# Optimization experiments

Measured on AMD Instinct MI355X. Metric: run time of the kernel, lower is better.

Reference implementation:

```python
import math
import jax, jax.numpy as jnp
import numpy as np

N_HEADS = 8
WINDOW = 4


def _get_relative_embeddings(emb, length, window):
    # emb: [1, 2*window+1, k_channels] -> [1, 2*length-1, k_channels]
    pad_length = max(length - (window + 1), 0)
    start = max(window + 1 - length, 0)
    if pad_length > 0:
        emb = jnp.pad(emb, ((0, 0), (pad_length, pad_length), (0, 0)))
    return emb[:, start:start + 2 * length - 1]


def _relative_position_to_absolute_position(x):
    # x: [b, h, l, 2l-1] -> [b, h, l, l] (skewing trick)
    b, h, l, _ = x.shape
    x = jnp.pad(x, ((0, 0), (0, 0), (0, 0), (0, 1)))
    x_flat = x.reshape(b, h, l * 2 * l)
    x_flat = jnp.pad(x_flat, ((0, 0), (0, 0), (0, l - 1)))
    return x_flat.reshape(b, h, l + 1, 2 * l - 1)[:, :, :l, l - 1:]


def _absolute_position_to_relative_position(x):
    # x: [b, h, l, l] -> [b, h, l, 2l-1]
    b, h, l, _ = x.shape
    x = jnp.pad(x, ((0, 0), (0, 0), (0, 0), (0, l - 1)))
    x_flat = x.reshape(b, h, l * l + l * (l - 1))
    x_flat = jnp.pad(x_flat, ((0, 0), (0, 0), (l, 0)))
    return x_flat.reshape(b, h, l, 2 * l)[:, :, :, 1:]


def setup_inputs() -> dict:
    key = jax.random.key(0)
    ks = jax.random.split(key, 12)
    b, t, d = 4, 1024, 512
    kc = d // N_HEADS
    s = 1.0 / math.sqrt(d)
    return {
        "x": jax.random.normal(ks[0], (b, t, d), jnp.float32),
        "c": jax.random.normal(ks[1], (b, t, d), jnp.float32),
        "wq": jax.random.normal(ks[2], (d, d), jnp.float32) * s,
        "bq": jnp.zeros((d,), jnp.float32),
        "wk": jax.random.normal(ks[3], (d, d), jnp.float32) * s,
        "bk": jnp.zeros((d,), jnp.float32),
        "wv": jax.random.normal(ks[4], (d, d), jnp.float32) * s,
        "bv": jnp.zeros((d,), jnp.float32),
        "wo": jax.random.normal(ks[5], (d, d), jnp.float32) * s,
        "bo": jnp.zeros((d,), jnp.float32),
        "emb_rel_k": jax.random.normal(ks[6], (1, 2 * WINDOW + 1, kc), jnp.float32) * kc ** -0.5,
        "emb_rel_v": jax.random.normal(ks[7], (1, 2 * WINDOW + 1, kc), jnp.float32) * kc ** -0.5,
    }


def reference(x, c, wq, bq, wk, bk, wv, bv, wo, bo, emb_rel_k, emb_rel_v):
    b, t, d = x.shape
    h = N_HEADS
    kc = d // h
    inv_sqrt = 1.0 / math.sqrt(kc)

    # 1x1 conv projections (pointwise matmul)
    q = x @ wq + bq   # [b, t, d]
    k = c @ wk + bk
    v = c @ wv + bv

    # Faithful reshape as in source: [b, t, d] -> [b, h, kc, t] -> [b, h, t, kc]
    q = q.reshape(b, h, kc, t).transpose(0, 1, 3, 2)
    k = k.reshape(b, h, kc, t).transpose(0, 1, 3, 2)
    v = v.reshape(b, h, kc, t).transpose(0, 1, 3, 2)

    scores = jnp.einsum('bhtd,bhsd->bhts', q, k) * inv_sqrt  # [b,h,t,t]

    # relative key logits
    key_rel = _get_relative_embeddings(emb_rel_k, t, WINDOW)[0]  # [2t-1, kc]
    rel_logits = jnp.einsum('bhtd,md->bhtm', q, key_rel)          # [b,h,t,2t-1]
    scores_local = _relative_position_to_absolute_position(rel_logits) * inv_sqrt
    scores = scores + scores_local

    p_attn = jax.nn.softmax(scores, axis=-1)
    output = jnp.einsum('bhts,bhsd->bhtd', p_attn, v)  # [b,h,t,kc]

    # relative value contribution
    rel_weights = _absolute_position_to_relative_position(p_attn)  # [b,h,t,2t-1]
    val_rel = _get_relative_embeddings(emb_rel_v, t, WINDOW)[0]    # [2t-1, kc]
    output = output + jnp.einsum('bhtm,md->bhtd', rel_weights, val_rel)

    # Faithful output reshape: [b,h,t,kc] -> [b,h,kc,t] -> [b,t,d]
    output = output.transpose(0, 1, 3, 2).reshape(b, t, d)
    out = output @ wo + bo
    return out
```

## Files before the change

kernel.cpp:

```cpp
#include <hip/hip_runtime.h>
#include <hip/hip_bf16.h>

#define NB 4
#define NT 1024
#define ND 512
#define NH 8
#define NKC 64

typedef __bf16 bf16x8 __attribute__((ext_vector_type(8)));
typedef float f32x4 __attribute__((ext_vector_type(4)));

__device__ __forceinline__ f32x4 MFMA(bf16x8 a, bf16x8 b, f32x4 c) {
    return __builtin_amdgcn_mfma_f32_16x16x32_bf16(a, b, c, 0, 0, 0);
}
__device__ __forceinline__ unsigned short f2bu(float v) {
    __hip_bfloat16 b = __float2bfloat16(v);
    return *(unsigned short*)&b;
}
__device__ __forceinline__ void split1(float v, unsigned short& h, unsigned short& l)
{
    __hip_bfloat16 hb = __float2bfloat16(v);
    float r = v - __bfloat162float(hb);
    __hip_bfloat16 lb = __float2bfloat16(r);
    h = *(unsigned short*)&hb;
    l = *(unsigned short*)&lb;
}
__device__ __forceinline__ void splitpack(const float4 a, const float4 b, uint4& h, uint4& l)
{
    union { unsigned short u[8]; uint4 v; } H, L;
    const float f[8] = {a.x, a.y, a.z, a.w, b.x, b.y, b.z, b.w};
    #pragma unroll
    for (int j = 0; j < 8; ++j) split1(f[j], H.u[j], L.u[j]);
    h = H.v; l = L.v;
}

__global__ __launch_bounds__(256)
void splitT_kernel(const float* __restrict__ w0, const float* __restrict__ w1,
                   const float* __restrict__ w2, const float* __restrict__ w3,
                   unsigned short* __restrict__ wT)
{
    __shared__ float tl[32][33];
    const float* w = (blockIdx.z == 0) ? w0 : (blockIdx.z == 1) ? w1
                   : (blockIdx.z == 2) ? w2 : w3;
    unsigned short* hi = wT + (size_t)blockIdx.z * 2 * (ND * ND);
    unsigned short* lo = hi + ND * ND;
    const int t = threadIdx.x;
    const int x0 = blockIdx.x * 32, y0 = blockIdx.y * 32;
    {
        const int r = t >> 3, c = (t & 7) * 4;
        const float4 v = *(const float4*)&w[(size_t)(y0 + r) * ND + x0 + c];
        tl[r][c] = v.x; tl[r][c+1] = v.y; tl[r][c+2] = v.z; tl[r][c+3] = v.w;
    }
    __syncthreads();
    {
        const int nr = t >> 3, k4 = (t & 7) * 4;
        unsigned short hh[4], ll[4];
        #pragma unroll
        for (int j = 0; j < 4; ++j) split1(tl[k4 + j][nr], hh[j], ll[j]);
        ushort4 h = make_ushort4(hh[0], hh[1], hh[2], hh[3]);
        ushort4 l = make_ushort4(ll[0], ll[1], ll[2], ll[3]);
        *(ushort4*)&hi[(size_t)(x0 + nr) * ND + y0 + k4] = h;
        *(ushort4*)&lo[(size_t)(x0 + nr) * ND + y0 + k4] = l;
    }
}

__global__ __launch_bounds__(256, 3)
void proj_mfma(const float* __restrict__ x, const float* __restrict__ cc,
               const unsigned short* __restrict__ wT,
               const float* __restrict__ bq, const float* __restrict__ bk,
               const float* __restrict__ bv,
               unsigned short* __restrict__ qh_o, unsigned short* __restrict__ ql_o,
               unsigned short* __restrict__ kh_o, unsigned short* __restrict__ vh_o)
{
    __shared__ unsigned short smem[12288];
    unsigned short* Ah = smem;
    unsigned short* Al = smem + 2048;
    unsigned short* Bh = smem + 4096;
    unsigned short* Bl = smem + 8192;
    unsigned short* Tr = smem;

    const int which = blockIdx.z;
    const float* A_g = (which == 0) ? x : cc;
    const unsigned short* Bh_g = wT + (size_t)which * 2 * (ND * ND);
    const unsigned short* Bl_g = Bh_g + ND * ND;
    const float* bias = (which == 0) ? bq : (which == 1) ? bk : bv;

    const int tid = threadIdx.x, l = tid & 63, w = tid >> 6;
    const int quad = l >> 4, lc = l & 15;
    const int wm = w & 1, wn = w >> 1;
    const int n0 = blockIdx.x * 128, m0 = blockIdx.y * 64;

    const int am = tid >> 2, ak = (tid & 3) * 8;
    const size_t aG = (size_t)(m0 + am) * ND + ak;
    const int bn = tid >> 1, bk2 = (tid & 1) * 16;
    const size_t bG = (size_t)(n0 + bn) * ND + bk2;

    float4 ra0 = *(const float4*)&A_g[aG];
    float4 ra1 = *(const float4*)&A_g[aG + 4];
    uint4 rb0 = *(const uint4*)&Bh_g[bG];
    uint4 rb1 = *(const uint4*)&Bh_g[bG + 8];
    uint4 rb2 = {}, rb3 = {};
    if (which != 2) {
        rb2 = *(const uint4*)&Bl_g[bG];
        rb3 = *(const uint4*)&Bl_g[bG + 8];
    }

    f32x4 acc[2][4];
    #pragma unroll
    for (int mi = 0; mi < 2; ++mi)
        #pragma unroll
        for (int ni = 0; ni < 4; ++ni) acc[mi][ni] = (f32x4){0.f, 0.f, 0.f, 0.f};

    for (int k0 = 0; k0 < ND; k0 += 32) {
        __syncthreads();
        {
            uint4 h0, l0;
            splitpack(ra0, ra1, h0, l0);
            *(uint4*)&Ah[am * 32 + ak] = h0;
            *(uint4*)&Al[am * 32 + ak] = l0;
            *(uint4*)&Bh[bn * 32 + bk2] = rb0; *(uint4*)&Bh[bn * 32 + bk2 + 8] = rb1;
            if (which != 2) {
                *(uint4*)&Bl[bn * 32 + bk2] = rb2; *(uint4*)&Bl[bn * 32 + bk2 + 8] = rb3;
            }
        }
        __syncthreads();
        if (k0 + 32 < ND) {
            const size_t aN = aG + k0 + 32, bN = bG + k0 + 32;
            ra0 = *(const float4*)&A_g[aN];
            ra1 = *(const float4*)&A_g[aN + 4];
            rb0 = *(const uint4*)&Bh_g[bN];
            rb1 = *(const uint4*)&Bh_g[bN + 8];
            if (which != 2) {
                rb2 = *(const uint4*)&Bl_g[bN];
                rb3 = *(const uint4*)&Bl_g[bN + 8];
            }
        }

        bf16x8 ah[2], al2[2], bh[4], bl[4];
        #pragma unroll
        for (int mi = 0; mi < 2; ++mi) {
            const int ar = (wm * 32 + mi * 16 + lc) * 32 + quad * 8;
            ah[mi] = *(const bf16x8*)&Ah[ar];
            al2[mi] = *(const bf16x8*)&Al[ar];
        }
        #pragma unroll
        for (int ni = 0; ni < 4; ++ni) {
            const int br = (wn * 64 + ni * 16 + lc) * 32 + quad * 8;
            bh[ni] = *(const bf16x8*)&Bh[br];
            if (which != 2) bl[ni] = *(const bf16x8*)&Bl[br];
        }
        if (which != 2) {
            #pragma unroll
            for (int mi = 0; mi < 2; ++mi)
                #pragma unroll
                for (int ni = 0; ni < 4; ++ni) {
                    acc[mi][ni] = MFMA(al2[mi], bh[ni], acc[mi][ni]);
                    acc[mi][ni] = MFMA(ah[mi], bl[ni], acc[mi][ni]);
                    acc[mi][ni] = MFMA(ah[mi], bh[ni], acc[mi][ni]);
                }
        } else {
            #pragma unroll
            for (int mi = 0; mi < 2; ++mi)
                #pragma unroll
                for (int ni = 0; ni < 4; ++ni) {
                    acc[mi][ni] = MFMA(al2[mi], bh[ni], acc[mi][ni]);
                    acc[mi][ni] = MFMA(ah[mi], bh[ni], acc[mi][ni]);
                }
        }
    }

    const int bb = m0 >> 10, tt0 = m0 & 1023;
    const int hh = tt0 >> 7, cch0 = (tt0 & 127) >> 1;
    const int bh_idx = bb * NH + hh;

    if (which == 2) {
        #pragma unroll
        for (int ni = 0; ni < 4; ++ni) {
            const int n = n0 + wn * 64 + ni * 16 + lc;
            const float bval = bias[n];
            #pragma unroll
            for (int mi = 0; mi < 2; ++mi)
                #pragma unroll
                for (int r = 0; r < 4; ++r) {
                    const int mloc = wm * 32 + mi * 16 + quad * 4 + r;
                    const int cch = cch0 + (mloc >> 1);
                    const int t = (mloc & 1) * 512 + n;
                    vh_o[(((size_t)bh_idx * 16 + (t >> 6)) * 64 + cch) * 64 + (t & 63)] =
                        f2bu(acc[mi][ni][r] + bval);
                }
        }
        return;
    }

    const int npass = (which == 0) ? 2 : 1;
    unsigned short* outp[2] = {(which == 0) ? qh_o : kh_o, ql_o};

    for (int pass = 0; pass < npass; ++pass) {
        __syncthreads();
        #pragma unroll
        for (int ni = 0; ni < 4; ++ni) {
            const int nloc = wn * 64 + ni * 16 + lc;
            const float bval = bias[n0 + nloc];
            #pragma unroll
            for (int mi = 0; mi < 2; ++mi)
                #pragma unroll
                for (int r = 0; r < 4; ++r) {
                    const int mloc = wm * 32 + mi * 16 + quad * 4 + r;
                    const float val = acc[mi][ni][r] + bval;
                    unsigned short hs, ls;
                    if (which == 0) { split1(val, hs, ls); }
                    else { hs = f2bu(val); ls = 0; }
                    Tr[((mloc & 1) * 128 + nloc) * 40 + (mloc >> 1)] =
                        (pass == 0) ? hs : ls;
                }
        }
        __syncthreads();
        {
            const int t = (tid >> 7) * 512 + n0 + (tid & 127);
            const size_t oa = ((size_t)bh_idx * NT + t) * NKC + cch0;
            const uint4 v0 = *(const uint4*)&Tr[tid * 40];
            const uint4 v1 = *(const uint4*)&Tr[tid * 40 + 8];
            const uint4 v2 = *(const uint4*)&Tr[tid * 40 + 16];
            const uint4 v3 = *(const uint4*)&Tr[tid * 40 + 24];
            *(uint4*)&outp[pass][oa]      = v0;
            *(uint4*)&outp[pass][oa + 8]  = v1;
            *(uint4*)&outp[pass][oa + 16] = v2;
            *(uint4*)&outp[pass][oa + 24] = v3;
        }
    }
}

__global__ __launch_bounds__(256, 4)
void attn_mfma(const unsigned short* __restrict__ qh_g, const unsigned short* __restrict__ ql_g,
               const unsigned short* __restrict__ kh_g,
               const unsigned short* __restrict__ vh_g,
               const float* __restrict__ embk, const float* __restrict__ embv,
               float* __restrict__ O0, float* __restrict__ O1,
               float* __restrict__ l0_g, float* __restrict__ l1_g)
{
    __shared__ unsigned short smem[19456];
    unsigned short* KsH = smem;
    unsigned short* Vt  = smem + 4608;
    unsigned short* Ps  = smem + 11264;
    float* bandv = (float*)(smem + 17920);
    unsigned short* EkH = smem + 11264;

    const int tid = threadIdx.x, l = tid & 63, w = tid >> 6;
    const int quad = l >> 4, lc = l & 15;
    const int q0 = (blockIdx.x >> 1) * 64;
    const int sh = blockIdx.x & 1;
    const int sBeg = sh * 512;
    const int hh = blockIdx.y, bb = blockIdx.z;
    const int bh = bb * NH + hh;
    const size_t qkBase = (size_t)bh * NT * NKC;
    const size_t vtBase = (size_t)bh * (16 * 64 * 64);
    float* Op = sh ? O1 : O0;
    float* lp = sh ? l1_g : l0_g;

    const int srow = tid >> 2, sseg = (tid & 3) * 16;

    auto loadKV = [&](uint4& k0r, uint4& k1r, uint4& v0r, uint4& v1r, int tile) {
        const size_t ka = qkBase + (size_t)(sBeg + tile * 64 + srow) * NKC + sseg;
        const size_t va = vtBase + (size_t)((sBeg >> 6) + tile) * 4096 + srow * 64 + sseg;
        k0r = *(const uint4*)&kh_g[ka];
        k1r = *(const uint4*)&kh_g[ka + 8];
        v0r = *(const uint4*)&vh_g[va];
        v1r = *(const uint4*)&vh_g[va + 8];
    };

    uint4 ak0, ak1, av0, av1, bk0, bk1, bv0, bv1;
    loadKV(ak0, ak1, av0, av1, 0);
    loadKV(bk0, bk1, bv0, bv1, 1);

    for (int idx = tid; idx < 16 * 72; idx += 256) {
        const int d = idx / 72, kc = idx - d * 72;
        EkH[idx] = f2bu((d < 9 && kc < 64) ? embk[d * 64 + kc] : 0.f);
    }
    for (int idx = tid; idx < 64 * 40; idx += 256) {
        const int c = idx / 40, col = 64 + (idx - c * 40);
        const int d = col - 64;
        Vt[c * 104 + col] = f2bu((d < 9) ? embv[d * 64 + c] : 0.f);
    }
    __syncthreads();

    bf16x8 qh[2], ql[2];
    {
        const int qg = q0 + w * 16 + lc;
        const size_t qa = qkBase + (size_t)qg * NKC + quad * 8;
        qh[0] = *(const bf16x8*)&qh_g[qa];
        qh[1] = *(const bf16x8*)&qh_g[qa + 32];
        ql[0] = *(const bf16x8*)&ql_g[qa];
        ql[1] = *(const bf16x8*)&ql_g[qa + 32];
    }

    {
        f32x4 accB = (f32x4){0.f, 0.f, 0.f, 0.f};
        #pragma unroll
        for (int kk = 0; kk < 2; ++kk) {
            const bf16x8 ebh = *(const bf16x8*)&EkH[lc * 72 + kk * 32 + quad * 8];
            accB = MFMA(ql[kk], ebh, accB);
            accB = MFMA(qh[kk], ebh, accB);
        }
        __syncthreads();
        if (lc <= 8) {
            #pragma unroll
            for (int r = 0; r < 4; ++r)
                bandv[(w * 16 + quad * 4 + r) * 12 + lc] = accB[r];
        }
    }
    unsigned short* P = Ps + w * 1664;
    {
        const int zr = l >> 2, zc = 80 + (l & 3) * 4;
        *(ushort4*)&P[zr * 104 + zc] = make_ushort4(0, 0, 0, 0);
    }

    f32x4 O[4];
    #pragma unroll
    for (int ci = 0; ci < 4; ++ci) O[ci] = (f32x4){0.f, 0.f, 0.f, 0.f};
    float l_run[4] = {0.f, 0.f, 0.f, 0.f};

    auto tilestep = [&](uint4& k0r, uint4& k1r, uint4& v0r, uint4& v1r,
                        int i, int nextTile) {
        const int s0 = sBeg + i * 64;
        __syncthreads();
        *(uint4*)&KsH[srow * 72 + sseg]      = k0r;
        *(uint4*)&KsH[srow * 72 + sseg + 8]  = k1r;
        *(uint4*)&Vt[srow * 104 + sseg]      = v0r;
        *(uint4*)&Vt[srow * 104 + sseg + 8]  = v1r;
        __syncthreads();
        if (nextTile >= 0) loadKV(k0r, k1r, v0r, v1r, nextTile);

        f32x4 S[4];
        #pragma unroll
        for (int ni = 0; ni < 4; ++ni) {
            f32x4 a = (f32x4){0.f, 0.f, 0.f, 0.f};
            #pragma unroll
            for (int kk = 0; kk < 2; ++kk) {
                const bf16x8 kb = *(const bf16x8*)&KsH[(ni * 16 + lc) * 72 + kk * 32 + quad * 8];
                a = MFMA(ql[kk], kb, a);
                a = MFMA(qh[kk], kb, a);
            }
            S[ni] = a;
        }

        #pragma unroll
        for (int ni = 0; ni < 4; ++ni)
            #pragma unroll
            for (int r = 0; r < 4; ++r) {
                const int ql64 = w * 16 + quad * 4 + r;
                const int dp4 = (s0 + ni * 16 + lc) - (q0 + ql64) + 4;
                float sv = S[ni][r];
                if (dp4 >= 0 && dp4 <= 8) sv += bandv[ql64 * 12 + dp4];
                S[ni][r] = __expf(sv * 0.125f);
            }
        #pragma unroll
        for (int r = 0; r < 4; ++r)
            l_run[r] += S[0][r] + S[1][r] + S[2][r] + S[3][r];

        {
            const int zr = l >> 2, zc = 64 + (l & 3) * 4;
            *(ushort4*)&P[zr * 104 + zc] = make_ushort4(0, 0, 0, 0);
        }
        #pragma unroll
        for (int ni = 0; ni < 4; ++ni)
            #pragma unroll
            for (int r = 0; r < 4; ++r) {
                const int prow = quad * 4 + r;
                const unsigned short pb = f2bu(S[ni][r]);
                P[prow * 104 + ni * 16 + lc] = pb;
                const int dp4 = (s0 + ni * 16 + lc) - (q0 + w * 16 + prow) + 4;
                if (dp4 >= 0 && dp4 <= 8) P[prow * 104 + 64 + dp4] = pb;
            }

        #pragma unroll
        for (int ks = 0; ks < 3; ++ks) {
            const bf16x8 pa = *(const bf16x8*)&P[lc * 104 + ks * 32 + quad * 8];
            #pragma unroll
            for (int ci = 0; ci < 4; ++ci) {
                const bf16x8 vb = *(const bf16x8*)&Vt[(ci * 16 + lc) * 104 + ks * 32 + quad * 8];
                O[ci] = MFMA(pa, vb, O[ci]);
            }
        }
    };

    for (int ii = 0; ii < 8; ii += 2) {
        tilestep(ak0, ak1, av0, av1, ii,     (ii + 2 < 8) ? ii + 2 : -1);
        tilestep(bk0, bk1, bv0, bv1, ii + 1, (ii + 3 < 8) ? ii + 3 : -1);
    }

    #pragma unroll
    for (int r = 0; r < 4; ++r) {
        float v = l_run[r];
        v += __shfl_xor(v, 1); v += __shfl_xor(v, 2);
        v += __shfl_xor(v, 4); v += __shfl_xor(v, 8);
        l_run[r] = v;
    }
    const int qg0 = q0 + w * 16 + quad * 4;
    if (lc == 0) {
        #pragma unroll
        for (int r = 0; r < 4; ++r)
            lp[(size_t)bh * NT + qg0 + r] = l_run[r];
    }
    #pragma unroll
    for (int ci = 0; ci < 4; ++ci) {
        const int c = ci * 16 + lc;
        *(f32x4*)&Op[((size_t)bh * 64 + c) * NT + qg0] = O[ci];
    }
}

__global__ __launch_bounds__(256, 4)
void outproj_fused(const float* __restrict__ O0, const float* __restrict__ O1,
                   const float* __restrict__ l0_g, const float* __restrict__ l1_g,
                   const unsigned short* __restrict__ wTh,
                   const float* __restrict__ bo, float* __restrict__ out)
{
    __shared__ unsigned short As[64 * 32], Bh[64 * 32], Bl[64 * 32];
    __shared__ float linv[1024];
    const unsigned short* Bl_g = wTh + ND * ND;
    const int tid = threadIdx.x, l = tid & 63, w = tid >> 6;
    const int quad = l >> 4, lc = l & 15;
    const int wm = w & 1, wn = w >> 1;
    const int n0 = blockIdx.x * 64, m0 = blockIdx.y * 64;

    const int bb = m0 >> 10, hh = (m0 & 1023) >> 7;
    const int bh = bb * NH + hh;

    for (int i = tid; i < 1024; i += 256)
        linv[i] = 1.f / (l0_g[(size_t)bh * NT + i] + l1_g[(size_t)bh * NT + i]);

    const int sm = tid >> 2, sk = (tid & 3) * 8;
    const int cch = ((m0 & 127) + sm) >> 1, tb = sm & 1;
    const size_t oBase = ((size_t)bh * 64 + cch) * NT + tb * 512 + sk;
    const size_t bG = (size_t)(n0 + sm) * ND + sk;

    float4 ro0a = *(const float4*)&O0[oBase];
    float4 ro0b = *(const float4*)&O0[oBase + 4];
    float4 ro1a = *(const float4*)&O1[oBase];
    float4 ro1b = *(const float4*)&O1[oBase + 4];
    uint4 rbh = *(const uint4*)&wTh[bG];
    uint4 rbl = *(const uint4*)&Bl_g[bG];

    f32x4 acc[2][2];
    #pragma unroll
    for (int mi = 0; mi < 2; ++mi)
        #pragma unroll
        for (int ni = 0; ni < 2; ++ni) acc[mi][ni] = (f32x4){0.f, 0.f, 0.f, 0.f};

    for (int k0 = 0; k0 < ND; k0 += 32) {
        __syncthreads();
        {
            const float* lv = &linv[tb * 512 + k0 + sk];
            const float f[8] = {ro0a.x + ro1a.x, ro0a.y + ro1a.y,
                                ro0a.z + ro1a.z, ro0a.w + ro1a.w,
                                ro0b.x + ro1b.x, ro0b.y + ro1b.y,
                                ro0b.z + ro1b.z, ro0b.w + ro1b.w};
            union { unsigned short u[8]; uint4 v; } pk;
            #pragma unroll
            for (int j = 0; j < 8; ++j) pk.u[j] = f2bu(f[j] * lv[j]);
            *(uint4*)&As[sm * 32 + sk] = pk.v;
            *(uint4*)&Bh[sm * 32 + sk] = rbh;
            *(uint4*)&Bl[sm * 32 + sk] = rbl;
        }
        __syncthreads();
        if (k0 + 32 < ND) {
            ro0a = *(const float4*)&O0[oBase + k0 + 32];
            ro0b = *(const float4*)&O0[oBase + k0 + 36];
            ro1a = *(const float4*)&O1[oBase + k0 + 32];
            ro1b = *(const float4*)&O1[oBase + k0 + 36];
            rbh  = *(const uint4*)&wTh[bG + k0 + 32];
            rbl  = *(const uint4*)&Bl_g[bG + k0 + 32];
        }
        bf16x8 ab[2], bhf[2], blf[2];
        #pragma unroll
        for (int mi = 0; mi < 2; ++mi)
            ab[mi] = *(const bf16x8*)&As[(wm * 32 + mi * 16 + lc) * 32 + quad * 8];
        #pragma unroll
        for (int ni = 0; ni < 2; ++ni) {
            const int br = (wn * 32 + ni * 16 + lc) * 32 + quad * 8;
            bhf[ni] = *(const bf16x8*)&Bh[br];
            blf[ni] = *(const bf16x8*)&Bl[br];
        }
        #pragma unroll
        for (int mi = 0; mi < 2; ++mi)
            #pragma unroll
            for (int ni = 0; ni < 2; ++ni) {
                acc[mi][ni] = MFMA(ab[mi], bhf[ni], acc[mi][ni]);
                acc[mi][ni] = MFMA(ab[mi], blf[ni], acc[mi][ni]);
            }
    }

    #pragma unroll
    for (int ni = 0; ni < 2; ++ni) {
        const int n = n0 + wn * 32 + ni * 16 + lc;
        const float bval = bo[n];
        #pragma unroll
        for (int mi = 0; mi < 2; ++mi)
            #pragma unroll
            for (int r = 0; r < 4; ++r) {
                const int m = m0 + wm * 32 + mi * 16 + quad * 4 + r;
                out[(size_t)m * ND + n] = acc[mi][ni][r] + bval;
            }
    }
}

extern "C" void kernel_launch(void* const* d_in, const int* in_sizes, int n_in,
                              void* d_out, int out_size, void* d_ws, size_t ws_size,
                              hipStream_t stream) {
    const float* x    = (const float*)d_in[0];
    const float* c    = (const float*)d_in[1];
    const float* wq   = (const float*)d_in[2];
    const float* bq   = (const float*)d_in[3];
    const float* wk   = (const float*)d_in[4];
    const float* bk   = (const float*)d_in[5];
    const float* wv   = (const float*)d_in[6];
    const float* bv   = (const float*)d_in[7];
    const float* wo   = (const float*)d_in[8];
    const float* bo   = (const float*)d_in[9];
    const float* embk = (const float*)d_in[10];
    const float* embv = (const float*)d_in[11];

    unsigned short* u16 = (unsigned short*)d_ws;
    const size_t M = 1024 * 1024;
    unsigned short* wT  = u16;
    unsigned short* qh  = u16 + 2 * M;
    unsigned short* ql  = u16 + 4 * M;
    unsigned short* kh  = u16 + 6 * M;
    unsigned short* vh  = u16 + 8 * M;
    float* fbase = (float*)(u16 + 10 * M);
    float* O0   = fbase;
    float* O1   = fbase + 2 * M;
    float* l0_g = fbase + 4 * M;
    float* l1_g = l0_g + 32768;

    splitT_kernel<<<dim3(16, 16, 4), 256, 0, stream>>>(wq, wk, wv, wo, wT);

    proj_mfma<<<dim3(4, 64, 3), 256, 0, stream>>>(x, c, wT, bq, bk, bv,
                                                  qh, ql, kh, vh);

    attn_mfma<<<dim3(32, 8, 4), 256, 0, stream>>>(qh, ql, kh, vh,
                                                  embk, embv, O0, O1, l0_g, l1_g);

    outproj_fused<<<dim3(8, 64), 256, 0, stream>>>(O0, O1, l0_g, l1_g,
                                                   wT + (size_t)3 * 2 * ND * ND,
                                                   bo, (float*)d_out);
}
```

Baseline: 171.1 us.

## Process 128 queries per attention block and split combine from output projection

```diff
diff --git a/kernel.cpp b/kernel.cpp
--- a/kernel.cpp
+++ b/kernel.cpp
@@ -230,7 +230,7 @@
     }
 }
 
-__global__ __launch_bounds__(256, 4)
+__global__ __launch_bounds__(256, 2)
 void attn_mfma(const unsigned short* __restrict__ qh_g, const unsigned short* __restrict__ ql_g,
                const unsigned short* __restrict__ kh_g,
                const unsigned short* __restrict__ vh_g,
@@ -238,7 +238,7 @@
                float* __restrict__ O0, float* __restrict__ O1,
                float* __restrict__ l0_g, float* __restrict__ l1_g)
 {
-    __shared__ unsigned short smem[19456];
+    __shared__ unsigned short smem[20992];
     unsigned short* KsH = smem;
     unsigned short* Vt  = smem + 4608;
     unsigned short* Ps  = smem + 11264;
@@ -247,7 +247,7 @@
 
     const int tid = threadIdx.x, l = tid & 63, w = tid >> 6;
     const int quad = l >> 4, lc = l & 15;
-    const int q0 = (blockIdx.x >> 1) * 64;
+    const int q0 = (blockIdx.x >> 1) * 128;
     const int sh = blockIdx.x & 1;
     const int sBeg = sh * 512;
     const int hh = blockIdx.y, bb = blockIdx.z;
@@ -283,29 +283,36 @@
     }
     __syncthreads();
 
-    bf16x8 qh[2], ql[2];
+    bf16x8 qh[2][2], ql[2][2];
+    #pragma unroll
+    for (int j = 0; j < 2; ++j) {
+        const int qg = q0 + j * 64 + w * 16 + lc;
+        const size_t qa = qkBase + (size_t)qg * NKC + quad * 8;
+        qh[j][0] = *(const bf16x8*)&qh_g[qa];
+        qh[j][1] = *(const bf16x8*)&qh_g[qa + 32];
+        ql[j][0] = *(const bf16x8*)&ql_g[qa];
+        ql[j][1] = *(const bf16x8*)&ql_g[qa + 32];
+    }
+
     {
-        const int qg = q0 + w * 16 + lc;
-        const size_t qa = qkBase + (size_t)qg * NKC + quad * 8;
-        qh[0] = *(const bf16x8*)&qh_g[qa];
-        qh[1] = *(const bf16x8*)&qh_g[qa + 32];
-        ql[0] = *(const bf16x8*)&ql_g[qa];
-        ql[1] = *(const bf16x8*)&ql_g[qa + 32];
-    }
-
-    {
-        f32x4 accB = (f32x4){0.f, 0.f, 0.f, 0.f};
-        #pragma unroll
-        for (int kk = 0; kk < 2; ++kk) {
-            const bf16x8 ebh = *(const bf16x8*)&EkH[lc * 72 + kk * 32 + quad * 8];
-            accB = MFMA(ql[kk], ebh, accB);
-            accB = MFMA(qh[kk], ebh, accB);
+        f32x4 accB[2];
+        #pragma unroll
+        for (int j = 0; j < 2; ++j) {
+            accB[j] = (f32x4){0.f, 0.f, 0.f, 0.f};
+            #pragma unroll
+            for (int kk = 0; kk < 2; ++kk) {
+                const bf16x8 ebh = *(const bf16x8*)&EkH[lc * 72 + kk * 32 + quad * 8];
+                accB[j] = MFMA(ql[j][kk], ebh, accB[j]);
+                accB[j] = MFMA(qh[j][kk], ebh, accB[j]);
+            }
         }
         __syncthreads();
         if (lc <= 8) {
             #pragma unroll
-            for (int r = 0; r < 4; ++r)
-                bandv[(w * 16 + quad * 4 + r) * 12 + lc] = accB[r];
+            for (int j = 0; j < 2; ++j)
+                #pragma unroll
+                for (int r = 0; r < 4; ++r)
+                    bandv[(j * 64 + w * 16 + quad * 4 + r) * 12 + lc] = accB[j][r];
         }
     }
     unsigned short* P = Ps + w * 1664;
@@ -314,10 +321,12 @@
         *(ushort4*)&P[zr * 104 + zc] = make_ushort4(0, 0, 0, 0);
     }
 
-    f32x4 O[4];
-    #pragma unroll
-    for (int ci = 0; ci < 4; ++ci) O[ci] = (f32x4){0.f, 0.f, 0.f, 0.f};
-    float l_run[4] = {0.f, 0.f, 0.f, 0.f};
+    f32x4 O[2][4];
+    #pragma unroll
+    for (int j = 0; j < 2; ++j)
+        #pragma unroll
+        for (int ci = 0; ci < 4; ++ci) O[j][ci] = (f32x4){0.f, 0.f, 0.f, 0.f};
+    float l_run[2][4] = {};
 
     auto tilestep = [&](uint4& k0r, uint4& k1r, uint4& v0r, uint4& v1r,
                         int i, int nextTile) {
@@ -330,55 +339,58 @@
         __syncthreads();
         if (nextTile >= 0) loadKV(k0r, k1r, v0r, v1r, nextTile);
 
-        f32x4 S[4];
-        #pragma unroll
-        for (int ni = 0; ni < 4; ++ni) {
-            f32x4 a = (f32x4){0.f, 0.f, 0.f, 0.f};
-            #pragma unroll
-            for (int kk = 0; kk < 2; ++kk) {
-                const bf16x8 kb = *(const bf16x8*)&KsH[(ni * 16 + lc) * 72 + kk * 32 + quad * 8];
-                a = MFMA(ql[kk], kb, a);
-                a = MFMA(qh[kk], kb, a);
-            }
-            S[ni] = a;
-        }
-
-        #pragma unroll
-        for (int ni = 0; ni < 4; ++ni)
-            #pragma unroll
-            for (int r = 0; r < 4; ++r) {
-                const int ql64 = w * 16 + quad * 4 + r;
-                const int dp4 = (s0 + ni * 16 + lc) - (q0 + ql64) + 4;
-                float sv = S[ni][r];
-                if (dp4 >= 0 && dp4 <= 8) sv += bandv[ql64 * 12 + dp4];
-                S[ni][r] = __expf(sv * 0.125f);
-            }
-        #pragma unroll
-        for (int r = 0; r < 4; ++r)
-            l_run[r] += S[0][r] + S[1][r] + S[2][r] + S[3][r];
-
-        {
-            const int zr = l >> 2, zc = 64 + (l & 3) * 4;
-            *(ushort4*)&P[zr * 104 + zc] = make_ushort4(0, 0, 0, 0);
-        }
-        #pragma unroll
-        for (int ni = 0; ni < 4; ++ni)
-            #pragma unroll
-            for (int r = 0; r < 4; ++r) {
-                const int prow = quad * 4 + r;
-                const unsigned short pb = f2bu(S[ni][r]);
-                P[prow * 104 + ni * 16 + lc] = pb;
-                const int dp4 = (s0 + ni * 16 + lc) - (q0 + w * 16 + prow) + 4;
-                if (dp4 >= 0 && dp4 <= 8) P[prow * 104 + 64 + dp4] = pb;
-            }
-
-        #pragma unroll
-        for (int ks = 0; ks < 3; ++ks) {
-            const bf16x8 pa = *(const bf16x8*)&P[lc * 104 + ks * 32 + quad * 8];
-            #pragma unroll
-            for (int ci = 0; ci < 4; ++ci) {
-                const bf16x8 vb = *(const bf16x8*)&Vt[(ci * 16 + lc) * 104 + ks * 32 + quad * 8];
-                O[ci] = MFMA(pa, vb, O[ci]);
+        #pragma unroll
+        for (int j = 0; j < 2; ++j) {
+            f32x4 S[4];
+            #pragma unroll
+            for (int ni = 0; ni < 4; ++ni) {
+                f32x4 a = (f32x4){0.f, 0.f, 0.f, 0.f};
+                #pragma unroll
+                for (int kk = 0; kk < 2; ++kk) {
+                    const bf16x8 kb = *(const bf16x8*)&KsH[(ni * 16 + lc) * 72 + kk * 32 + quad * 8];
+                    a = MFMA(ql[j][kk], kb, a);
+                    a = MFMA(qh[j][kk], kb, a);
+                }
+                S[ni] = a;
+            }
+
+            #pragma unroll
+            for (int ni = 0; ni < 4; ++ni)
+                #pragma unroll
+                for (int r = 0; r < 4; ++r) {
+                    const int ql128 = j * 64 + w * 16 + quad * 4 + r;
+                    const int dp4 = (s0 + ni * 16 + lc) - (q0 + ql128) + 4;
+                    float sv = S[ni][r];
+                    if (dp4 >= 0 && dp4 <= 8) sv += bandv[ql128 * 12 + dp4];
+                    S[ni][r] = __expf(sv * 0.125f);
+                }
+            #pragma unroll
+            for (int r = 0; r < 4; ++r)
+                l_run[j][r] += S[0][r] + S[1][r] + S[2][r] + S[3][r];
+
+            {
+                const int zr = l >> 2, zc = 64 + (l & 3) * 4;
+                *(ushort4*)&P[zr * 104 + zc] = make_ushort4(0, 0, 0, 0);
+            }
+            #pragma unroll
+            for (int ni = 0; ni < 4; ++ni)
+                #pragma unroll
+                for (int r = 0; r < 4; ++r) {
+                    const int prow = quad * 4 + r;
+                    const unsigned short pb = f2bu(S[ni][r]);
+                    P[prow * 104 + ni * 16 + lc] = pb;
+                    const int dp4 = (s0 + ni * 16 + lc) - (q0 + j * 64 + w * 16 + prow) + 4;
+                    if (dp4 >= 0 && dp4 <= 8) P[prow * 104 + 64 + dp4] = pb;
+                }
+
+            #pragma unroll
+            for (int ks = 0; ks < 3; ++ks) {
+                const bf16x8 pa = *(const bf16x8*)&P[lc * 104 + ks * 32 + quad * 8];
+                #pragma unroll
+                for (int ci = 0; ci < 4; ++ci) {
+                    const bf16x8 vb = *(const bf16x8*)&Vt[(ci * 16 + lc) * 104 + ks * 32 + quad * 8];
+                    O[j][ci] = MFMA(pa, vb, O[j][ci]);
+                }
             }
         }
     };
@@ -388,55 +400,87 @@
         tilestep(bk0, bk1, bv0, bv1, ii + 1, (ii + 3 < 8) ? ii + 3 : -1);
     }
 
-    #pragma unroll
-    for (int r = 0; r < 4; ++r) {
-        float v = l_run[r];
-        v += __shfl_xor(v, 1); v += __shfl_xor(v, 2);
-        v += __shfl_xor(v, 4); v += __shfl_xor(v, 8);
-        l_run[r] = v;
-    }
-    const int qg0 = q0 + w * 16 + quad * 4;
-    if (lc == 0) {
+    float* Os = (float*)smem;
+    #pragma unroll
+    for (int j = 0; j < 2; ++j) {
+        #pragma unroll
+        for (int r = 0; r < 4; ++r) {
+            float v = l_run[j][r];
+            v += __shfl_xor(v, 1); v += __shfl_xor(v, 2);
+            v += __shfl_xor(v, 4); v += __shfl_xor(v, 8);
+            l_run[j][r] = v;
+        }
+        const int qg0 = q0 + j * 64 + w * 16 + quad * 4;
+        if (lc == 0) {
+            #pragma unroll
+            for (int r = 0; r < 4; ++r)
+                lp[(size_t)bh * NT + qg0 + r] = l_run[j][r];
+        }
+        __syncthreads();
+        #pragma unroll
+        for (int ci = 0; ci < 4; ++ci)
+            #pragma unroll
+            for (int r = 0; r < 4; ++r)
+                Os[(ci * 16 + lc) * 68 + w * 16 + quad * 4 + r] = O[j][ci][r];
+        __syncthreads();
+        {
+            const int c = tid >> 2, q4 = (tid & 3) * 16;
+            const size_t ob = ((size_t)bh * 64 + c) * NT + q0 + j * 64 + q4;
+            #pragma unroll
+            for (int i4 = 0; i4 < 16; i4 += 4)
+                *(f32x4*)&Op[ob + i4] = *(const f32x4*)&Os[c * 68 + q4 + i4];
+        }
+    }
+}
+
+__global__ __launch_bounds__(256)
+void combine_kernel(const float* __restrict__ O0, const float* __restrict__ O1,
+                    const float* __restrict__ l0_g, const float* __restrict__ l1_g,
+                    unsigned short* __restrict__ ath)
+{
+    const int q0 = blockIdx.x * 64, hh = blockIdx.y, bb = blockIdx.z;
+    const int bh = bb * NH + hh;
+    const int tid = threadIdx.x;
+    __shared__ float linv[64];
+    if (tid < 64)
+        linv[tid] = 1.f / (l0_g[(size_t)bh * NT + q0 + tid] +
+                           l1_g[(size_t)bh * NT + q0 + tid]);
+    __syncthreads();
+
+    const int c = tid >> 2, qq = (tid & 3) * 16;
+    const size_t ib = ((size_t)bh * 64 + c) * NT + q0 + qq;
+    union { unsigned short u[16]; uint4 v[2]; } out;
+    #pragma unroll
+    for (int j = 0; j < 16; j += 4) {
+        const f32x4 a = *(const f32x4*)&O0[ib + j];
+        const f32x4 b = *(const f32x4*)&O1[ib + j];
         #pragma unroll
         for (int r = 0; r < 4; ++r)
-            lp[(size_t)bh * NT + qg0 + r] = l_run[r];
-    }
-    #pragma unroll
-    for (int ci = 0; ci < 4; ++ci) {
-        const int c = ci * 16 + lc;
-        *(f32x4*)&Op[((size_t)bh * 64 + c) * NT + qg0] = O[ci];
-    }
+            out.u[j + r] = f2bu((a[r] + b[r]) * linv[qq + j + r]);
+    }
+    const int row = hh * 128 + 2 * c + (q0 >> 9);
+    const size_t oa = ((size_t)bb * NT + row) * ND + (q0 & 511) + qq;
+    *(uint4*)&ath[oa]     = out.v[0];
+    *(uint4*)&ath[oa + 8] = out.v[1];
 }
 
 __global__ __launch_bounds__(256, 4)
-void outproj_fused(const float* __restrict__ O0, const float* __restrict__ O1,
-                   const float* __restrict__ l0_g, const float* __restrict__ l1_g,
-                   const unsigned short* __restrict__ wTh,
-                   const float* __restrict__ bo, float* __restrict__ out)
+void outproj_mfma(const unsigned short* __restrict__ a_g,
+                  const unsigned short* __restrict__ wTh,
+                  const float* __restrict__ bo, float* __restrict__ out)
 {
     __shared__ unsigned short As[64 * 32], Bh[64 * 32], Bl[64 * 32];
-    __shared__ float linv[1024];
     const unsigned short* Bl_g = wTh + ND * ND;
     const int tid = threadIdx.x, l = tid & 63, w = tid >> 6;
     const int quad = l >> 4, lc = l & 15;
     const int wm = w & 1, wn = w >> 1;
     const int n0 = blockIdx.x * 64, m0 = blockIdx.y * 64;
 
-    const int bb = m0 >> 10, hh = (m0 & 1023) >> 7;
-    const int bh = bb * NH + hh;
-
-    for (int i = tid; i < 1024; i += 256)
-        linv[i] = 1.f / (l0_g[(size_t)bh * NT + i] + l1_g[(size_t)bh * NT + i]);
-
     const int sm = tid >> 2, sk = (tid & 3) * 8;
-    const int cch = ((m0 & 127) + sm) >> 1, tb = sm & 1;
-    const size_t oBase = ((size_t)bh * 64 + cch) * NT + tb * 512 + sk;
+    const size_t aG = (size_t)(m0 + sm) * ND + sk;
     const size_t bG = (size_t)(n0 + sm) * ND + sk;
 
-    float4 ro0a = *(const float4*)&O0[oBase];
-    float4 ro0b = *(const float4*)&O0[oBase + 4];
-    float4 ro1a = *(const float4*)&O1[oBase];
-    float4 ro1b = *(const float4*)&O1[oBase + 4];
+    uint4 ra  = *(const uint4*)&a_g[aG];
     uint4 rbh = *(const uint4*)&wTh[bG];
     uint4 rbl = *(const uint4*)&Bl_g[bG];
 
@@ -448,27 +492,14 @@
 
     for (int k0 = 0; k0 < ND; k0 += 32) {
         __syncthreads();
-        {
-            const float* lv = &linv[tb * 512 + k0 + sk];
-            const float f[8] = {ro0a.x + ro1a.x, ro0a.y + ro1a.y,
-                                ro0a.z + ro1a.z, ro0a.w + ro1a.w,
-                                ro0b.x + ro1b.x, ro0b.y + ro1b.y,
-                                ro0b.z + ro1b.z, ro0b.w + ro1b.w};
-            union { unsigned short u[8]; uint4 v; } pk;
-            #pragma unroll
-            for (int j = 0; j < 8; ++j) pk.u[j] = f2bu(f[j] * lv[j]);
-            *(uint4*)&As[sm * 32 + sk] = pk.v;
-            *(uint4*)&Bh[sm * 32 + sk] = rbh;
-            *(uint4*)&Bl[sm * 32 + sk] = rbl;
-        }
+        *(uint4*)&As[sm * 32 + sk] = ra;
+        *(uint4*)&Bh[sm * 32 + sk] = rbh;
+        *(uint4*)&Bl[sm * 32 + sk] = rbl;
         __syncthreads();
         if (k0 + 32 < ND) {
-            ro0a = *(const float4*)&O0[oBase + k0 + 32];
-            ro0b = *(const float4*)&O0[oBase + k0 + 36];
-            ro1a = *(const float4*)&O1[oBase + k0 + 32];
-            ro1b = *(const float4*)&O1[oBase + k0 + 36];
-            rbh  = *(const uint4*)&wTh[bG + k0 + 32];
-            rbl  = *(const uint4*)&Bl_g[bG + k0 + 32];
+            ra  = *(const uint4*)&a_g[aG + k0 + 32];
+            rbh = *(const uint4*)&wTh[bG + k0 + 32];
+            rbl = *(const uint4*)&Bl_g[bG + k0 + 32];
         }
         bf16x8 ab[2], bhf[2], blf[2];
         #pragma unroll
@@ -526,7 +557,8 @@
     unsigned short* ql  = u16 + 4 * M;
     unsigned short* kh  = u16 + 6 * M;
     unsigned short* vh  = u16 + 8 * M;
-    float* fbase = (float*)(u16 + 10 * M);
+    unsigned short* ath = u16 + 10 * M;
+    float* fbase = (float*)(u16 + 12 * M);
     float* O0   = fbase;
     float* O1   = fbase + 2 * M;
     float* l0_g = fbase + 4 * M;
@@ -537,10 +569,12 @@
     proj_mfma<<<dim3(4, 64, 3), 256, 0, stream>>>(x, c, wT, bq, bk, bv,
                                                   qh, ql, kh, vh);
 
-    attn_mfma<<<dim3(32, 8, 4), 256, 0, stream>>>(qh, ql, kh, vh,
+    attn_mfma<<<dim3(16, 8, 4), 256, 0, stream>>>(qh, ql, kh, vh,
                                                   embk, embv, O0, O1, l0_g, l1_g);
 
-    outproj_fused<<<dim3(8, 64), 256, 0, stream>>>(O0, O1, l0_g, l1_g,
-                                                   wT + (size_t)3 * 2 * ND * ND,
-                                                   bo, (float*)d_out);
-}
+    combine_kernel<<<dim3(16, 8, 4), 256, 0, stream>>>(O0, O1, l0_g, l1_g, ath);
+
+    outproj_mfma<<<dim3(8, 64), 256, 0, stream>>>(ath,
+                                                  wT + (size_t)3 * 2 * ND * ND,
+                                                  bo, (float*)d_out);
+}
```

After: 171.1 us. About the same (-0.0%).

## Fuse output projection into attention kernel with atomic accumulation

Applied to the files above, without the earlier changes.

```diff
diff --git a/kernel.cpp b/kernel.cpp
--- a/kernel.cpp
+++ b/kernel.cpp
@@ -32,6 +32,14 @@
     #pragma unroll
     for (int j = 0; j < 8; ++j) split1(f[j], H.u[j], L.u[j]);
     h = H.v; l = L.v;
+}
+
+__global__ __launch_bounds__(256)
+void init_out(const float* __restrict__ bo, float* __restrict__ out)
+{
+    const int idx = blockIdx.x * 256 + threadIdx.x;
+    const float4 b4 = *(const float4*)&bo[(idx & 127) * 4];
+    *(float4*)&out[(size_t)idx * 4] = b4;
 }
 
 __global__ __launch_bounds__(256)
@@ -230,38 +238,38 @@
     }
 }
 
-__global__ __launch_bounds__(256, 4)
-void attn_mfma(const unsigned short* __restrict__ qh_g, const unsigned short* __restrict__ ql_g,
-               const unsigned short* __restrict__ kh_g,
-               const unsigned short* __restrict__ vh_g,
-               const float* __restrict__ embk, const float* __restrict__ embv,
-               float* __restrict__ O0, float* __restrict__ O1,
-               float* __restrict__ l0_g, float* __restrict__ l1_g)
-{
-    __shared__ unsigned short smem[19456];
+__global__ __launch_bounds__(256, 2)
+void attn_fused(const unsigned short* __restrict__ qh_g, const unsigned short* __restrict__ ql_g,
+                const unsigned short* __restrict__ kh_g,
+                const unsigned short* __restrict__ vh_g,
+                const float* __restrict__ embk, const float* __restrict__ embv,
+                const unsigned short* __restrict__ woT,
+                float* __restrict__ out)
+{
+    __shared__ unsigned short smem[23040];
     unsigned short* KsH = smem;
     unsigned short* Vt  = smem + 4608;
     unsigned short* Ps  = smem + 11264;
     float* bandv = (float*)(smem + 17920);
     unsigned short* EkH = smem + 11264;
-
-    const int tid = threadIdx.x, l = tid & 63, w = tid >> 6;
+    unsigned short* OnT  = smem;
+    unsigned short* BstH = smem + 4608;
+    unsigned short* BstL = smem + 13824;
+
+    const int tid = threadIdx.x, l = tid & 63, wv = tid >> 6;
     const int quad = l >> 4, lc = l & 15;
-    const int q0 = (blockIdx.x >> 1) * 64;
-    const int sh = blockIdx.x & 1;
-    const int sBeg = sh * 512;
+    const int q0 = blockIdx.x * 64;
     const int hh = blockIdx.y, bb = blockIdx.z;
     const int bh = bb * NH + hh;
+    const int thi = q0 >> 9, tl0 = q0 & 511;
     const size_t qkBase = (size_t)bh * NT * NKC;
     const size_t vtBase = (size_t)bh * (16 * 64 * 64);
-    float* Op = sh ? O1 : O0;
-    float* lp = sh ? l1_g : l0_g;
 
     const int srow = tid >> 2, sseg = (tid & 3) * 16;
 
     auto loadKV = [&](uint4& k0r, uint4& k1r, uint4& v0r, uint4& v1r, int tile) {
-        const size_t ka = qkBase + (size_t)(sBeg + tile * 64 + srow) * NKC + sseg;
-        const size_t va = vtBase + (size_t)((sBeg >> 6) + tile) * 4096 + srow * 64 + sseg;
+        const size_t ka = qkBase + (size_t)(tile * 64 + srow) * NKC + sseg;
+        const size_t va = vtBase + (size_t)tile * 4096 + srow * 64 + sseg;
         k0r = *(const uint4*)&kh_g[ka];
         k1r = *(const uint4*)&kh_g[ka + 8];
         v0r = *(const uint4*)&vh_g[va];
@@ -285,7 +293,7 @@
 
     bf16x8 qh[2], ql[2];
     {
-        const int qg = q0 + w * 16 + lc;
+        const int qg = q0 + wv * 16 + lc;
         const size_t qa = qkBase + (size_t)qg * NKC + quad * 8;
         qh[0] = *(const bf16x8*)&qh_g[qa];
         qh[1] = *(const bf16x8*)&qh_g[qa + 32];
@@ -305,10 +313,10 @@
         if (lc <= 8) {
             #pragma unroll
             for (int r = 0; r < 4; ++r)
-                bandv[(w * 16 + quad * 4 + r) * 12 + lc] = accB[r];
-        }
-    }
-    unsigned short* P = Ps + w * 1664;
+                bandv[(wv * 16 + quad * 4 + r) * 12 + lc] = accB[r];
+        }
+    }
+    unsigned short* P = Ps + wv * 1664;
     {
         const int zr = l >> 2, zc = 80 + (l & 3) * 4;
         *(ushort4*)&P[zr * 104 + zc] = make_ushort4(0, 0, 0, 0);
@@ -321,7 +329,7 @@
 
     auto tilestep = [&](uint4& k0r, uint4& k1r, uint4& v0r, uint4& v1r,
                         int i, int nextTile) {
-        const int s0 = sBeg + i * 64;
+        const int s0 = i * 64;
         __syncthreads();
         *(uint4*)&KsH[srow * 72 + sseg]      = k0r;
         *(uint4*)&KsH[srow * 72 + sseg + 8]  = k1r;
@@ -347,7 +355,7 @@
         for (int ni = 0; ni < 4; ++ni)
             #pragma unroll
             for (int r = 0; r < 4; ++r) {
-                const int ql64 = w * 16 + quad * 4 + r;
+                const int ql64 = wv * 16 + quad * 4 + r;
                 const int dp4 = (s0 + ni * 16 + lc) - (q0 + ql64) + 4;
                 float sv = S[ni][r];
                 if (dp4 >= 0 && dp4 <= 8) sv += bandv[ql64 * 12 + dp4];
@@ -368,7 +376,7 @@
                 const int prow = quad * 4 + r;
                 const unsigned short pb = f2bu(S[ni][r]);
                 P[prow * 104 + ni * 16 + lc] = pb;
-                const int dp4 = (s0 + ni * 16 + lc) - (q0 + w * 16 + prow) + 4;
+                const int dp4 = (s0 + ni * 16 + lc) - (q0 + wv * 16 + prow) + 4;
                 if (dp4 >= 0 && dp4 <= 8) P[prow * 104 + 64 + dp4] = pb;
             }
 
@@ -383,9 +391,9 @@
         }
     };
 
-    for (int ii = 0; ii < 8; ii += 2) {
-        tilestep(ak0, ak1, av0, av1, ii,     (ii + 2 < 8) ? ii + 2 : -1);
-        tilestep(bk0, bk1, bv0, bv1, ii + 1, (ii + 3 < 8) ? ii + 3 : -1);
+    for (int ii = 0; ii < 16; ii += 2) {
+        tilestep(ak0, ak1, av0, av1, ii,     (ii + 2 < 16) ? ii + 2 : -1);
+        tilestep(bk0, bk1, bv0, bv1, ii + 1, (ii + 3 < 16) ? ii + 3 : -1);
     }
 
     #pragma unroll
@@ -393,113 +401,58 @@
         float v = l_run[r];
         v += __shfl_xor(v, 1); v += __shfl_xor(v, 2);
         v += __shfl_xor(v, 4); v += __shfl_xor(v, 8);
-        l_run[r] = v;
-    }
-    const int qg0 = q0 + w * 16 + quad * 4;
-    if (lc == 0) {
+        l_run[r] = 1.f / v;
+    }
+
+    __syncthreads();
+    #pragma unroll
+    for (int ci = 0; ci < 4; ++ci)
         #pragma unroll
         for (int r = 0; r < 4; ++r)
-            lp[(size_t)bh * NT + qg0 + r] = l_run[r];
-    }
-    #pragma unroll
-    for (int ci = 0; ci < 4; ++ci) {
-        const int c = ci * 16 + lc;
-        *(f32x4*)&Op[((size_t)bh * 64 + c) * NT + qg0] = O[ci];
-    }
-}
-
-__global__ __launch_bounds__(256, 4)
-void outproj_fused(const float* __restrict__ O0, const float* __restrict__ O1,
-                   const float* __restrict__ l0_g, const float* __restrict__ l1_g,
-                   const unsigned short* __restrict__ wTh,
-                   const float* __restrict__ bo, float* __restrict__ out)
-{
-    __shared__ unsigned short As[64 * 32], Bh[64 * 32], Bl[64 * 32];
-    __shared__ float linv[1024];
-    const unsigned short* Bl_g = wTh + ND * ND;
-    const int tid = threadIdx.x, l = tid & 63, w = tid >> 6;
-    const int quad = l >> 4, lc = l & 15;
-    const int wm = w & 1, wn = w >> 1;
-    const int n0 = blockIdx.x * 64, m0 = blockIdx.y * 64;
-
-    const int bb = m0 >> 10, hh = (m0 & 1023) >> 7;
-    const int bh = bb * NH + hh;
-
-    for (int i = tid; i < 1024; i += 256)
-        linv[i] = 1.f / (l0_g[(size_t)bh * NT + i] + l1_g[(size_t)bh * NT + i]);
-
-    const int sm = tid >> 2, sk = (tid & 3) * 8;
-    const int cch = ((m0 & 127) + sm) >> 1, tb = sm & 1;
-    const size_t oBase = ((size_t)bh * 64 + cch) * NT + tb * 512 + sk;
-    const size_t bG = (size_t)(n0 + sm) * ND + sk;
-
-    float4 ro0a = *(const float4*)&O0[oBase];
-    float4 ro0b = *(const float4*)&O0[oBase + 4];
-    float4 ro1a = *(const float4*)&O1[oBase];
-    float4 ro1b = *(const float4*)&O1[oBase + 4];
-    uint4 rbh = *(const uint4*)&wTh[bG];
-    uint4 rbl = *(const uint4*)&Bl_g[bG];
-
-    f32x4 acc[2][2];
-    #pragma unroll
-    for (int mi = 0; mi < 2; ++mi)
-        #pragma unroll
-        for (int ni = 0; ni < 2; ++ni) acc[mi][ni] = (f32x4){0.f, 0.f, 0.f, 0.f};
-
-    for (int k0 = 0; k0 < ND; k0 += 32) {
-        __syncthreads();
+            OnT[(ci * 16 + lc) * 72 + wv * 16 + quad * 4 + r] =
+                f2bu(O[ci][r] * l_run[r]);
+
+    const unsigned short* woT_l = woT + ND * ND;
+    const int br2 = tid >> 1, bs2 = (tid & 1) * 32;
+
+    for (int nc = 0; nc < 4; ++nc) {
         {
-            const float* lv = &linv[tb * 512 + k0 + sk];
-            const float f[8] = {ro0a.x + ro1a.x, ro0a.y + ro1a.y,
-                                ro0a.z + ro1a.z, ro0a.w + ro1a.w,
-                                ro0b.x + ro1b.x, ro0b.y + ro1b.y,
-                                ro0b.z + ro1b.z, ro0b.w + ro1b.w};
-            union { unsigned short u[8]; uint4 v; } pk;
-            #pragma unroll
-            for (int j = 0; j < 8; ++j) pk.u[j] = f2bu(f[j] * lv[j]);
-            *(uint4*)&As[sm * 32 + sk] = pk.v;
-            *(uint4*)&Bh[sm * 32 + sk] = rbh;
-            *(uint4*)&Bl[sm * 32 + sk] = rbl;
-        }
-        __syncthreads();
-        if (k0 + 32 < ND) {
-            ro0a = *(const float4*)&O0[oBase + k0 + 32];
-            ro0b = *(const float4*)&O0[oBase + k0 + 36];
-            ro1a = *(const float4*)&O1[oBase + k0 + 32];
-            ro1b = *(const float4*)&O1[oBase + k0 + 36];
-            rbh  = *(const uint4*)&wTh[bG + k0 + 32];
-            rbl  = *(const uint4*)&Bl_g[bG + k0 + 32];
-        }
-        bf16x8 ab[2], bhf[2], blf[2];
-        #pragma unroll
-        for (int mi = 0; mi < 2; ++mi)
-            ab[mi] = *(const bf16x8*)&As[(wm * 32 + mi * 16 + lc) * 32 + quad * 8];
-        #pragma unroll
-        for (int ni = 0; ni < 2; ++ni) {
-            const int br = (wn * 32 + ni * 16 + lc) * 32 + quad * 8;
-            bhf[ni] = *(const bf16x8*)&Bh[br];
-            blf[ni] = *(const bf16x8*)&Bl[br];
-        }
-        #pragma unroll
-        for (int mi = 0; mi < 2; ++mi)
-            #pragma unroll
-            for (int ni = 0; ni < 2; ++ni) {
-                acc[mi][ni] = MFMA(ab[mi], bhf[ni], acc[mi][ni]);
-                acc[mi][ni] = MFMA(ab[mi], blf[ni], acc[mi][ni]);
-            }
-    }
-
-    #pragma unroll
-    for (int ni = 0; ni < 2; ++ni) {
-        const int n = n0 + wn * 32 + ni * 16 + lc;
-        const float bval = bo[n];
-        #pragma unroll
-        for (int mi = 0; mi < 2; ++mi)
+            const size_t wbase = (size_t)(nc * 128 + br2) * ND + tl0 + bs2;
+            #pragma unroll
+            for (int j = 0; j < 32; j += 8) {
+                *(uint4*)&BstH[br2 * 72 + bs2 + j] = *(const uint4*)&woT[wbase + j];
+                *(uint4*)&BstL[br2 * 72 + bs2 + j] = *(const uint4*)&woT_l[wbase + j];
+            }
+        }
+        __syncthreads();
+
+        bf16x8 af[2];
+        af[0] = *(const bf16x8*)&OnT[(wv * 16 + lc) * 72 + quad * 8];
+        af[1] = *(const bf16x8*)&OnT[(wv * 16 + lc) * 72 + 32 + quad * 8];
+
+        f32x4 acc[8];
+        #pragma unroll
+        for (int ni = 0; ni < 8; ++ni) acc[ni] = (f32x4){0.f, 0.f, 0.f, 0.f};
+        #pragma unroll
+        for (int ni = 0; ni < 8; ++ni)
+            #pragma unroll
+            for (int kk = 0; kk < 2; ++kk) {
+                const int br = (ni * 16 + lc) * 72 + kk * 32 + quad * 8;
+                acc[ni] = MFMA(af[kk], *(const bf16x8*)&BstH[br], acc[ni]);
+                acc[ni] = MFMA(af[kk], *(const bf16x8*)&BstL[br], acc[ni]);
+            }
+
+        #pragma unroll
+        for (int ni = 0; ni < 8; ++ni) {
+            const int n = nc * 128 + ni * 16 + lc;
             #pragma unroll
             for (int r = 0; r < 4; ++r) {
-                const int m = m0 + wm * 32 + mi * 16 + quad * 4 + r;
-                out[(size_t)m * ND + n] = acc[mi][ni][r] + bval;
-            }
+                const int c = wv * 16 + quad * 4 + r;
+                const int irow = hh * 128 + 2 * c + thi;
+                atomicAdd(&out[((size_t)(bb * NT + irow)) * ND + n], acc[ni][r]);
+            }
+        }
+        __syncthreads();
     }
 }
 
@@ -521,26 +474,20 @@
 
     unsigned short* u16 = (unsigned short*)d_ws;
     const size_t M = 1024 * 1024;
-    unsigned short* wT  = u16;
-    unsigned short* qh  = u16 + 2 * M;
-    unsigned short* ql  = u16 + 4 * M;
-    unsigned short* kh  = u16 + 6 * M;
-    unsigned short* vh  = u16 + 8 * M;
-    float* fbase = (float*)(u16 + 10 * M);
-    float* O0   = fbase;
-    float* O1   = fbase + 2 * M;
-    float* l0_g = fbase + 4 * M;
-    float* l1_g = l0_g + 32768;
+    unsigned short* wT = u16;
+    unsigned short* qh = u16 + 2 * M;
+    unsigned short* ql = u16 + 4 * M;
+    unsigned short* kh = u16 + 6 * M;
+    unsigned short* vh = u16 + 8 * M;
 
     splitT_kernel<<<dim3(16, 16, 4), 256, 0, stream>>>(wq, wk, wv, wo, wT);
+
+    init_out<<<(NB * NT * ND / 4) / 256, 256, 0, stream>>>(bo, (float*)d_out);
 
     proj_mfma<<<dim3(4, 64, 3), 256, 0, stream>>>(x, c, wT, bq, bk, bv,
                                                   qh, ql, kh, vh);
 
-    attn_mfma<<<dim3(32, 8, 4), 256, 0, stream>>>(qh, ql, kh, vh,
-                                                  embk, embv, O0, O1, l0_g, l1_g);
-
-    outproj_fused<<<dim3(8, 64), 256, 0, stream>>>(O0, O1, l0_g, l1_g,
+    attn_fused<<<dim3(16, 8, 4), 256, 0, stream>>>(qh, ql, kh, vh, embk, embv,
                                                    wT + (size_t)3 * 2 * ND * ND,
-                                                   bo, (float*)d_out);
-}
+                                                   (float*)d_out);
+}
```

New measurement: 200.0 us. +16.9%, slower.
